# Kernel tuning notes

Measured on AMD Instinct MI355X. Metric: run time of the kernel, lower is better.

## Reference

```python
import jax, jax.numpy as jnp
import numpy as np

EPS = 1e-5

def sage_conv(x, edge_index, w_l, b_l, w_r):
    # PyG SAGEConv with mean aggregation: lin_l(mean of source-neighbor feats per dst) + lin_r(x)
    n = x.shape[0]
    src, dst = edge_index[0], edge_index[1]
    agg = jax.ops.segment_sum(x[src], dst, num_segments=n)  # [N, d]
    deg = jax.ops.segment_sum(jnp.ones((edge_index.shape[1],), x.dtype), dst, num_segments=n)
    agg = agg / jnp.maximum(deg, 1.0)[:, None]
    return agg @ w_l + b_l + x @ w_r

def batchnorm_eval(x, gamma, beta, mean, var):
    return (x - mean) * (gamma * jax.lax.rsqrt(var + EPS)) + beta

def setup_inputs() -> dict:
    key = jax.random.key(0)
    ks = jax.random.split(key, 12)
    N, E, D, H, O = 10000, 160000, 512, 512, 256
    inp = {
        'x': jax.random.normal(ks[0], (N, D), jnp.float32),
        'edge_index': jax.random.randint(ks[1], (2, E), 0, N, jnp.int32),
        'w_l1': jax.random.normal(ks[2], (D, H), jnp.float32) * (1.0 / np.sqrt(D)),
        'b1': jnp.zeros((H,), jnp.float32),
        'w_r1': jax.random.normal(ks[3], (D, H), jnp.float32) * (1.0 / np.sqrt(D)),
        'bn1_gamma': jnp.ones((H,), jnp.float32),
        'bn1_beta': jnp.zeros((H,), jnp.float32),
        'bn1_mean': jax.random.normal(ks[4], (H,), jnp.float32) * 0.1,
        'bn1_var': jax.random.uniform(ks[5], (H,), jnp.float32, 0.5, 1.5),
        'w_l2': jax.random.normal(ks[6], (H, H), jnp.float32) * (1.0 / np.sqrt(H)),
        'b2': jnp.zeros((H,), jnp.float32),
        'w_r2': jax.random.normal(ks[7], (H, H), jnp.float32) * (1.0 / np.sqrt(H)),
        'bn2_gamma': jnp.ones((H,), jnp.float32),
        'bn2_beta': jnp.zeros((H,), jnp.float32),
        'bn2_mean': jax.random.normal(ks[8], (H,), jnp.float32) * 0.1,
        'bn2_var': jax.random.uniform(ks[9], (H,), jnp.float32, 0.5, 1.5),
        'w_l3': jax.random.normal(ks[10], (H, O), jnp.float32) * (1.0 / np.sqrt(H)),
        'b3': jnp.zeros((O,), jnp.float32),
        'w_r3': jax.random.normal(ks[11], (H, O), jnp.float32) * (1.0 / np.sqrt(H)),
    }
    return inp

def reference(x, edge_index, w_l1, b1, w_r1, bn1_gamma, bn1_beta, bn1_mean, bn1_var,
              w_l2, b2, w_r2, bn2_gamma, bn2_beta, bn2_mean, bn2_var,
              w_l3, b3, w_r3):
    # Layer 1: SAGEConv -> BN (eval) -> ReLU (dropout is identity in eval)
    h = sage_conv(x, edge_index, w_l1, b1, w_r1)
    h = jax.nn.relu(batchnorm_eval(h, bn1_gamma, bn1_beta, bn1_mean, bn1_var))
    # Layer 2
    h = sage_conv(h, edge_index, w_l2, b2, w_r2)
    h = jax.nn.relu(batchnorm_eval(h, bn2_gamma, bn2_beta, bn2_mean, bn2_var))
    # Layer 3 (no BN/ReLU)
    return sage_conv(h, edge_index, w_l3, b3, w_r3)
```

## Files before the change

kernel.cpp:

```cpp
#include <hip/hip_runtime.h>

#define NNODE 10000
#define NEDGE 160000

using frag8 = __attribute__((ext_vector_type(8))) short;
using f32x4 = __attribute__((ext_vector_type(4))) float;

__device__ __forceinline__ unsigned short f2bf(float f) {
    union { float f; unsigned u; } v; v.f = f;
    unsigned r = (v.u + 0x7fffu + ((v.u >> 16) & 1u)) >> 16;
    return (unsigned short)r;
}
__device__ __forceinline__ float bf2f(unsigned short s) {
    union { unsigned u; float f; } v; v.u = ((unsigned)s) << 16; return v.f;
}

__global__ __launch_bounds__(1024) void k_scan(const int* __restrict__ deg,
                                               int* __restrict__ rs,
                                               int* __restrict__ cur, int n, int total) {
    const int tid = threadIdx.x;
    const int CH = 10;
    const int base = tid * CH;
    int vals[CH];
    int tsum = 0;
#pragma unroll
    for (int j = 0; j < CH; j++) {
        int v = (base + j < n) ? deg[base + j] : 0;
        vals[j] = v; tsum += v;
    }
    const int lane = tid & 63, wid = tid >> 6;
    int x = tsum;
#pragma unroll
    for (int d = 1; d < 64; d <<= 1) {
        int y = __shfl_up(x, d, 64);
        if (lane >= d) x += y;
    }
    __shared__ int wt[16];
    if (lane == 63) wt[wid] = x;
    __syncthreads();
    if (tid == 0) {
        int c = 0;
#pragma unroll
        for (int k = 0; k < 16; k++) { int t = wt[k]; wt[k] = c; c += t; }
    }
    __syncthreads();
    int run = wt[wid] + x - tsum;
#pragma unroll
    for (int j = 0; j < CH; j++) {
        if (base + j < n) { rs[base + j] = run; cur[base + j] = run; }
        run += vals[j];
    }
    if (tid == 0) rs[n] = total;
}

__global__ void k_fill(const int* __restrict__ src, const int* __restrict__ dst,
                       int E, int* __restrict__ cur, int* __restrict__ csr) {
    int e = blockIdx.x * 256 + threadIdx.x;
    if (e < E) {
        int p = atomicAdd(&cur[dst[e]], 1);
        csr[p] = src[e];
    }
}

__global__ __launch_bounds__(256) void k_prep(
    const float* __restrict__ x, unsigned short* __restrict__ xb,
    const float* __restrict__ wl1, const float* __restrict__ wr1,
    const float* __restrict__ wl2, const float* __restrict__ wr2,
    const float* __restrict__ wl3, const float* __restrict__ wr3,
    unsigned short* __restrict__ bt1, unsigned short* __restrict__ bt2,
    unsigned short* __restrict__ bt3,
    const float* __restrict__ b1, const float* __restrict__ g1, const float* __restrict__ be1,
    const float* __restrict__ m1, const float* __restrict__ v1,
    const float* __restrict__ b2, const float* __restrict__ g2, const float* __restrict__ be2,
    const float* __restrict__ m2, const float* __restrict__ v2,
    const float* __restrict__ b3,
    float* __restrict__ sc1, float* __restrict__ sh1,
    float* __restrict__ sc2, float* __restrict__ sh2,
    float* __restrict__ sc3, float* __restrict__ sh3,
    const int* __restrict__ dstI, int* __restrict__ deg) {
    const int b = blockIdx.x, tid = threadIdx.x;
    if (b < 5000) {
        int i = b * 256 + tid;
        float4 f = ((const float4*)x)[i];
        ushort4 o;
        o.x = f2bf(f.x); o.y = f2bf(f.y); o.z = f2bf(f.z); o.w = f2bf(f.w);
        ((ushort4*)xb)[i] = o;
        return;
    }
    if (b >= 6281) {
        int e = (b - 6281) * 256 + tid;
        if (e < NEDGE) atomicAdd(&deg[dstI[e]], 1);
        return;
    }
    if (b == 6280) {
        for (int t = tid; t < 512; t += 256) {
            float s1 = g1[t] * rsqrtf(v1[t] + 1e-5f);
            sc1[t] = s1; sh1[t] = (b1[t] - m1[t]) * s1 + be1[t];
            float s2 = g2[t] * rsqrtf(v2[t] + 1e-5f);
            sc2[t] = s2; sh2[t] = (b2[t] - m2[t]) * s2 + be2[t];
        }
        if (tid < 256) { sc3[tid] = 1.0f; sh3[tid] = b3[tid]; }
        return;
    }
    __shared__ float t[32][33];
    int tj = b - 5000;
    const float* srcp; unsigned short* dstp; int C, koff, ntilesN;
    if (tj < 1024) {
        int job = tj >> 8; int tile = tj & 255; C = 512; ntilesN = 16;
        srcp = (job == 0) ? wl1 : (job == 1) ? wr1 : (job == 2) ? wl2 : wr2;
        dstp = (job < 2) ? bt1 : bt2; koff = (job & 1) * 512;
        tj = tile;
    } else {
        int jj = tj - 1024; int job = jj >> 7; int tile = jj & 127; C = 256; ntilesN = 8;
        srcp = (job == 0) ? wl3 : wr3; dstp = bt3; koff = job * 512;
        tj = tile;
    }
    int k0 = (tj / ntilesN) * 32, c0 = (tj % ntilesN) * 32;
    int tx = tid & 31, ty = tid >> 5;
#pragma unroll
    for (int q = 0; q < 4; q++)
        t[ty + 8 * q][tx] = srcp[(long)(k0 + ty + 8 * q) * C + c0 + tx];
    __syncthreads();
#pragma unroll
    for (int q = 0; q < 4; q++)
        dstp[(long)(c0 + ty + 8 * q) * 1024 + koff + k0 + tx] = f2bf(t[tx][ty + 8 * q]);
}

__global__ __launch_bounds__(64) void k_agg(const unsigned short* __restrict__ S,
                                            const int* __restrict__ rs, const int* __restrict__ csr,
                                            unsigned short* __restrict__ outb) {
    const int n = blockIdx.x;
    const int c = blockIdx.y * 128 + threadIdx.x * 2;
    const int s = rs[n], e = rs[n + 1];
    float a0 = 0.f, a1 = 0.f;
    int i = s;
    for (; i + 4 <= e; i += 4) {
        int r0 = csr[i], r1 = csr[i + 1], r2 = csr[i + 2], r3 = csr[i + 3];
        unsigned u0 = *(const unsigned*)(S + (long)r0 * 512 + c);
        unsigned u1 = *(const unsigned*)(S + (long)r1 * 512 + c);
        unsigned u2 = *(const unsigned*)(S + (long)r2 * 512 + c);
        unsigned u3 = *(const unsigned*)(S + (long)r3 * 512 + c);
        a0 += bf2f((unsigned short)(u0 & 0xffffu)); a1 += bf2f((unsigned short)(u0 >> 16));
        a0 += bf2f((unsigned short)(u1 & 0xffffu)); a1 += bf2f((unsigned short)(u1 >> 16));
        a0 += bf2f((unsigned short)(u2 & 0xffffu)); a1 += bf2f((unsigned short)(u2 >> 16));
        a0 += bf2f((unsigned short)(u3 & 0xffffu)); a1 += bf2f((unsigned short)(u3 >> 16));
    }
    for (; i < e; i++) {
        unsigned u = *(const unsigned*)(S + (long)csr[i] * 512 + c);
        a0 += bf2f((unsigned short)(u & 0xffffu)); a1 += bf2f((unsigned short)(u >> 16));
    }
    const int cnt = e - s;
    const float inv = 1.f / (float)(cnt > 1 ? cnt : 1);
    unsigned o = (unsigned)f2bf(a0 * inv) | ((unsigned)f2bf(a1 * inv) << 16);
    *(unsigned*)(outb + (long)n * 512 + c) = o;
}

template <int MODE, int NOUT>
__global__ __launch_bounds__(256) void k_gemm(const unsigned short* __restrict__ Agg,
                                              const unsigned short* __restrict__ Self,
                                              const unsigned short* __restrict__ Bt,
                                              const float* __restrict__ sc, const float* __restrict__ sh,
                                              unsigned short* __restrict__ hout, float* __restrict__ fout,
                                              int M) {
    __shared__ __align__(16) short As[2][128 * 64];
    __shared__ __align__(16) short Bs[2][64 * 64];
    const int tid = threadIdx.x;
    const int m0 = blockIdx.x * 128, n0 = blockIdx.y * 64;
    const int w = tid >> 6, lane = tid & 63;
    const int wm = (w >> 1) * 64, wn = (w & 1) * 32;
    const int fr = lane & 15;
    const int fq = lane >> 4;
    const int sw = fr & 7;

    const int srow = w * 8 + (lane >> 3);
    const int scol = (((lane & 7) ^ (lane >> 3)) * 8);
    const int ldsOff = w * 8 * 64;

    f32x4 acc[4][2];
#pragma unroll
    for (int i = 0; i < 4; i++)
#pragma unroll
        for (int j = 0; j < 2; j++)
#pragma unroll
            for (int r = 0; r < 4; r++) acc[i][j][r] = 0.f;

    auto issue = [&](int t, int buf) {
        const short* abase = (const short*)((t < 8) ? Agg : Self);
        const int kk = (t & 7) * 64;
        const int k0 = t * 64;
#pragma unroll
        for (int cch = 0; cch < 4; cch++)
            __builtin_amdgcn_global_load_lds(
                (const __attribute__((address_space(1))) void*)(abase + (long)(m0 + cch * 32 + srow) * 512 + kk + scol),
                (__attribute__((address_space(3))) void*)(&As[buf][ldsOff + cch * 32 * 64]), 16, 0, 0);
#pragma unroll
        for (int cch = 0; cch < 2; cch++)
            __builtin_amdgcn_global_load_lds(
                (const __attribute__((address_space(1))) void*)((const short*)Bt + (long)(n0 + cch * 32 + srow) * 1024 + k0 + scol),
                (__attribute__((address_space(3))) void*)(&Bs[buf][ldsOff + cch * 32 * 64]), 16, 0, 0);
    };

    issue(0, 0);
#pragma unroll
    for (int t = 0; t < 16; t++) {
        const int cur = t & 1;
        __syncthreads();
        if (t < 15) issue(t + 1, cur ^ 1);
#pragma unroll
        for (int ks = 0; ks < 2; ks++) {
            frag8 af[4], bf[2];
#pragma unroll
            for (int i = 0; i < 4; i++)
                af[i] = *(const frag8*)(&As[cur][(wm + i * 16 + fr) * 64 + (((ks * 4 + fq) ^ sw) * 8)]);
#pragma unroll
            for (int j = 0; j < 2; j++)
                bf[j] = *(const frag8*)(&Bs[cur][(wn + j * 16 + fr) * 64 + (((ks * 4 + fq) ^ sw) * 8)]);
#pragma unroll
            for (int i = 0; i < 4; i++)
#pragma unroll
                for (int j = 0; j < 2; j++)
                    acc[i][j] = __builtin_amdgcn_mfma_f32_16x16x32_bf16(af[i], bf[j], acc[i][j], 0, 0, 0);
        }
        __syncthreads();
    }

    float scj[2], shj[2];
#pragma unroll
    for (int j = 0; j < 2; j++) {
        int col = n0 + wn + j * 16 + fr;
        scj[j] = sc[col]; shj[j] = sh[col];
    }
#pragma unroll
    for (int i = 0; i < 4; i++) {
        int rowb = m0 + wm + i * 16 + fq * 4;
#pragma unroll
        for (int j = 0; j < 2; j++) {
            int col = n0 + wn + j * 16 + fr;
#pragma unroll
            for (int r = 0; r < 4; r++) {
                int row = rowb + r;
                if (row < M) {
                    float y = acc[i][j][r] * scj[j] + shj[j];
                    if constexpr (MODE == 0) {
                        y = fmaxf(y, 0.f);
                        hout[(long)row * 512 + col] = f2bf(y);
                    } else {
                        fout[(long)row * NOUT + col] = y;
                    }
                }
            }
        }
    }
}

extern "C" void kernel_launch(void* const* d_in, const int* in_sizes, int n_in,
                              void* d_out, int out_size, void* d_ws, size_t ws_size,
                              hipStream_t stream) {
    const float* x    = (const float*)d_in[0];
    const int*   ei   = (const int*)d_in[1];
    const float* w_l1 = (const float*)d_in[2];
    const float* b1   = (const float*)d_in[3];
    const float* w_r1 = (const float*)d_in[4];
    const float* g1   = (const float*)d_in[5];
    const float* be1  = (const float*)d_in[6];
    const float* m1   = (const float*)d_in[7];
    const float* v1   = (const float*)d_in[8];
    const float* w_l2 = (const float*)d_in[9];
    const float* b2   = (const float*)d_in[10];
    const float* w_r2 = (const float*)d_in[11];
    const float* g2   = (const float*)d_in[12];
    const float* be2  = (const float*)d_in[13];
    const float* m2   = (const float*)d_in[14];
    const float* v2   = (const float*)d_in[15];
    const float* w_l3 = (const float*)d_in[16];
    const float* b3   = (const float*)d_in[17];
    const float* w_r3 = (const float*)d_in[18];
    float* out = (float*)d_out;

    const int N = NNODE, E = NEDGE;
    const int* srcI = ei;
    const int* dstI = ei + E;

    char* w = (char*)d_ws;
    auto alloc = [&](size_t bytes) { void* p = (void*)w; w += (bytes + 255) & ~(size_t)255; return p; };
    int* deg = (int*)alloc((size_t)N * 4);
    int* rs  = (int*)alloc((size_t)(N + 1) * 4);
    int* cur = (int*)alloc((size_t)N * 4);
    int* csr = (int*)alloc((size_t)E * 4);
    unsigned short* xb   = (unsigned short*)alloc((size_t)N * 512 * 2);
    unsigned short* bt1  = (unsigned short*)alloc((size_t)512 * 1024 * 2);
    unsigned short* bt2  = (unsigned short*)alloc((size_t)512 * 1024 * 2);
    unsigned short* bt3  = (unsigned short*)alloc((size_t)256 * 1024 * 2);
    float* sc1 = (float*)alloc(512 * 4); float* sh1 = (float*)alloc(512 * 4);
    float* sc2 = (float*)alloc(512 * 4); float* sh2 = (float*)alloc(512 * 4);
    float* sc3 = (float*)alloc(256 * 4); float* sh3 = (float*)alloc(256 * 4);
    unsigned short* agg_a = (unsigned short*)alloc((size_t)N * 512 * 2);
    unsigned short* h1    = (unsigned short*)alloc((size_t)N * 512 * 2);
    unsigned short* h2    = (unsigned short*)alloc((size_t)N * 512 * 2);
    (void)alloc(256 * 1024);

    hipMemsetAsync(deg, 0, (size_t)N * 4, stream);
    k_prep<<<6906, 256, 0, stream>>>(x, xb, w_l1, w_r1, w_l2, w_r2, w_l3, w_r3,
                                     bt1, bt2, bt3,
                                     b1, g1, be1, m1, v1, b2, g2, be2, m2, v2, b3,
                                     sc1, sh1, sc2, sh2, sc3, sh3, dstI, deg);
    k_scan<<<1, 1024, 0, stream>>>(deg, rs, cur, N, E);
    k_fill<<<(E + 255) / 256, 256, 0, stream>>>(srcI, dstI, E, cur, csr);

    dim3 g12((N + 127) / 128, 8);
    dim3 g3((N + 127) / 128, 4);
    dim3 ga(N, 4);

    k_agg<<<ga, 64, 0, stream>>>(xb, rs, csr, agg_a);
    k_gemm<0, 512><<<g12, 256, 0, stream>>>(agg_a, xb, bt1, sc1, sh1, h1, nullptr, N);
    k_agg<<<ga, 64, 0, stream>>>(h1, rs, csr, agg_a);
    k_gemm<0, 512><<<g12, 256, 0, stream>>>(agg_a, h1, bt2, sc2, sh2, h2, nullptr, N);
    k_agg<<<ga, 64, 0, stream>>>(h2, rs, csr, agg_a);
    k_gemm<1, 256><<<g3, 256, 0, stream>>>(agg_a, h2, bt3, sc3, sh3, nullptr, out, N);
}
```

Before: 272.5 us.

## Fuse all stages into one persistent cooperative kernel with grid syncs

Replaces the memset plus nine separate launches (prep, scan, fill, three aggregations, three GEMMs) with a single persistent cooperative kernel of 512 blocks that loops over work and separates phases with grid-wide barriers. Degree counting moves into its own phase after zeroing, the scan runs on one 256-thread block, and GEMM tiles are remapped in groups of 8 row tiles per column tile for L2 reuse. This removes launch gaps and per-kernel tail effects, but in exchange it limits parallelism to the resident grid and adds grid.sync overhead. The scan is now serialized on a single block while the rest of the grid waits.

After: 964.7 us. 254% more time.

```diff
diff --git a/kernel.cpp b/kernel.cpp
--- a/kernel.cpp
+++ b/kernel.cpp
@@ -1,7 +1,11 @@
 #include <hip/hip_runtime.h>
+#include <hip/hip_cooperative_groups.h>
+namespace cg = cooperative_groups;
 
 #define NNODE 10000
 #define NEDGE 160000
+#define GRID  512
+#define NTHR  256
 
 using frag8 = __attribute__((ext_vector_type(8))) short;
 using f32x4 = __attribute__((ext_vector_type(4))) float;
@@ -15,237 +19,153 @@
     union { unsigned u; float f; } v; v.u = ((unsigned)s) << 16; return v.f;
 }
 
-__global__ __launch_bounds__(1024) void k_scan(const int* __restrict__ deg,
-                                               int* __restrict__ rs,
-                                               int* __restrict__ cur, int n, int total) {
+struct P {
+    const float* x; const int* srcI; const int* dstI;
+    const float *wl1, *wr1, *wl2, *wr2, *wl3, *wr3;
+    const float *b1, *g1, *be1, *m1, *v1;
+    const float *b2, *g2, *be2, *m2, *v2;
+    const float *b3;
+    int *deg, *rs, *cur, *csr;
+    unsigned short *xb, *bt1, *bt2, *bt3, *agg, *h1, *h2;
+    float *sc1, *sh1, *sc2, *sh2, *sc3, *sh3;
+    float* out;
+};
+
+__device__ __forceinline__ void agg_phase(const unsigned short* __restrict__ S,
+                                          const int* __restrict__ rs,
+                                          const int* __restrict__ csr,
+                                          unsigned short* __restrict__ outb) {
+    const int lane = threadIdx.x & 63;
+    const int wv = blockIdx.x * 4 + (threadIdx.x >> 6);
+    for (int job = wv; job < 4 * NNODE; job += GRID * 4) {
+        const int pass = job / NNODE;
+        const int n = job - pass * NNODE;
+        const int c = pass * 128 + lane * 2;
+        const int s = rs[n], e = rs[n + 1];
+        float a0 = 0.f, a1 = 0.f;
+        int i = s;
+        for (; i + 4 <= e; i += 4) {
+            int r0 = csr[i], r1 = csr[i + 1], r2 = csr[i + 2], r3 = csr[i + 3];
+            unsigned u0 = *(const unsigned*)(S + (long)r0 * 512 + c);
+            unsigned u1 = *(const unsigned*)(S + (long)r1 * 512 + c);
+            unsigned u2 = *(const unsigned*)(S + (long)r2 * 512 + c);
+            unsigned u3 = *(const unsigned*)(S + (long)r3 * 512 + c);
+            a0 += bf2f((unsigned short)(u0 & 0xffffu)); a1 += bf2f((unsigned short)(u0 >> 16));
+            a0 += bf2f((unsigned short)(u1 & 0xffffu)); a1 += bf2f((unsigned short)(u1 >> 16));
+            a0 += bf2f((unsigned short)(u2 & 0xffffu)); a1 += bf2f((unsigned short)(u2 >> 16));
+            a0 += bf2f((unsigned short)(u3 & 0xffffu)); a1 += bf2f((unsigned short)(u3 >> 16));
+        }
+        for (; i < e; i++) {
+            unsigned u = *(const unsigned*)(S + (long)csr[i] * 512 + c);
+            a0 += bf2f((unsigned short)(u & 0xffffu)); a1 += bf2f((unsigned short)(u >> 16));
+        }
+        const int cnt = e - s;
+        const float inv = 1.f / (float)(cnt > 1 ? cnt : 1);
+        unsigned o = (unsigned)f2bf(a0 * inv) | ((unsigned)f2bf(a1 * inv) << 16);
+        *(unsigned*)(outb + (long)n * 512 + c) = o;
+    }
+}
+
+__device__ __forceinline__ void gemm_phase(const unsigned short* __restrict__ Agg,
+                                           const unsigned short* __restrict__ Self,
+                                           const unsigned short* __restrict__ Bt,
+                                           const float* __restrict__ sc, const float* __restrict__ sh,
+                                           unsigned short* __restrict__ hout, float* __restrict__ fout,
+                                           int NT, int qsh, int mode,
+                                           short* __restrict__ AsB, short* __restrict__ BsB) {
     const int tid = threadIdx.x;
-    const int CH = 10;
-    const int base = tid * CH;
-    int vals[CH];
-    int tsum = 0;
-#pragma unroll
-    for (int j = 0; j < CH; j++) {
-        int v = (base + j < n) ? deg[base + j] : 0;
-        vals[j] = v; tsum += v;
-    }
-    const int lane = tid & 63, wid = tid >> 6;
-    int x = tsum;
-#pragma unroll
-    for (int d = 1; d < 64; d <<= 1) {
-        int y = __shfl_up(x, d, 64);
-        if (lane >= d) x += y;
-    }
-    __shared__ int wt[16];
-    if (lane == 63) wt[wid] = x;
-    __syncthreads();
-    if (tid == 0) {
-        int c = 0;
-#pragma unroll
-        for (int k = 0; k < 16; k++) { int t = wt[k]; wt[k] = c; c += t; }
-    }
-    __syncthreads();
-    int run = wt[wid] + x - tsum;
-#pragma unroll
-    for (int j = 0; j < CH; j++) {
-        if (base + j < n) { rs[base + j] = run; cur[base + j] = run; }
-        run += vals[j];
-    }
-    if (tid == 0) rs[n] = total;
-}
-
-__global__ void k_fill(const int* __restrict__ src, const int* __restrict__ dst,
-                       int E, int* __restrict__ cur, int* __restrict__ csr) {
-    int e = blockIdx.x * 256 + threadIdx.x;
-    if (e < E) {
-        int p = atomicAdd(&cur[dst[e]], 1);
-        csr[p] = src[e];
-    }
-}
-
-__global__ __launch_bounds__(256) void k_prep(
-    const float* __restrict__ x, unsigned short* __restrict__ xb,
-    const float* __restrict__ wl1, const float* __restrict__ wr1,
-    const float* __restrict__ wl2, const float* __restrict__ wr2,
-    const float* __restrict__ wl3, const float* __restrict__ wr3,
-    unsigned short* __restrict__ bt1, unsigned short* __restrict__ bt2,
-    unsigned short* __restrict__ bt3,
-    const float* __restrict__ b1, const float* __restrict__ g1, const float* __restrict__ be1,
-    const float* __restrict__ m1, const float* __restrict__ v1,
-    const float* __restrict__ b2, const float* __restrict__ g2, const float* __restrict__ be2,
-    const float* __restrict__ m2, const float* __restrict__ v2,
-    const float* __restrict__ b3,
-    float* __restrict__ sc1, float* __restrict__ sh1,
-    float* __restrict__ sc2, float* __restrict__ sh2,
-    float* __restrict__ sc3, float* __restrict__ sh3,
-    const int* __restrict__ dstI, int* __restrict__ deg) {
-    const int b = blockIdx.x, tid = threadIdx.x;
-    if (b < 5000) {
-        int i = b * 256 + tid;
-        float4 f = ((const float4*)x)[i];
-        ushort4 o;
-        o.x = f2bf(f.x); o.y = f2bf(f.y); o.z = f2bf(f.z); o.w = f2bf(f.w);
-        ((ushort4*)xb)[i] = o;
-        return;
-    }
-    if (b >= 6281) {
-        int e = (b - 6281) * 256 + tid;
-        if (e < NEDGE) atomicAdd(&deg[dstI[e]], 1);
-        return;
-    }
-    if (b == 6280) {
-        for (int t = tid; t < 512; t += 256) {
-            float s1 = g1[t] * rsqrtf(v1[t] + 1e-5f);
-            sc1[t] = s1; sh1[t] = (b1[t] - m1[t]) * s1 + be1[t];
-            float s2 = g2[t] * rsqrtf(v2[t] + 1e-5f);
-            sc2[t] = s2; sh2[t] = (b2[t] - m2[t]) * s2 + be2[t];
-        }
-        if (tid < 256) { sc3[tid] = 1.0f; sh3[tid] = b3[tid]; }
-        return;
-    }
-    __shared__ float t[32][33];
-    int tj = b - 5000;
-    const float* srcp; unsigned short* dstp; int C, koff, ntilesN;
-    if (tj < 1024) {
-        int job = tj >> 8; int tile = tj & 255; C = 512; ntilesN = 16;
-        srcp = (job == 0) ? wl1 : (job == 1) ? wr1 : (job == 2) ? wl2 : wr2;
-        dstp = (job < 2) ? bt1 : bt2; koff = (job & 1) * 512;
-        tj = tile;
-    } else {
-        int jj = tj - 1024; int job = jj >> 7; int tile = jj & 127; C = 256; ntilesN = 8;
-        srcp = (job == 0) ? wl3 : wr3; dstp = bt3; koff = job * 512;
-        tj = tile;
-    }
-    int k0 = (tj / ntilesN) * 32, c0 = (tj % ntilesN) * 32;
-    int tx = tid & 31, ty = tid >> 5;
-#pragma unroll
-    for (int q = 0; q < 4; q++)
-        t[ty + 8 * q][tx] = srcp[(long)(k0 + ty + 8 * q) * C + c0 + tx];
-    __syncthreads();
-#pragma unroll
-    for (int q = 0; q < 4; q++)
-        dstp[(long)(c0 + ty + 8 * q) * 1024 + koff + k0 + tx] = f2bf(t[tx][ty + 8 * q]);
-}
-
-__global__ __launch_bounds__(64) void k_agg(const unsigned short* __restrict__ S,
-                                            const int* __restrict__ rs, const int* __restrict__ csr,
-                                            unsigned short* __restrict__ outb) {
-    const int n = blockIdx.x;
-    const int c = blockIdx.y * 128 + threadIdx.x * 2;
-    const int s = rs[n], e = rs[n + 1];
-    float a0 = 0.f, a1 = 0.f;
-    int i = s;
-    for (; i + 4 <= e; i += 4) {
-        int r0 = csr[i], r1 = csr[i + 1], r2 = csr[i + 2], r3 = csr[i + 3];
-        unsigned u0 = *(const unsigned*)(S + (long)r0 * 512 + c);
-        unsigned u1 = *(const unsigned*)(S + (long)r1 * 512 + c);
-        unsigned u2 = *(const unsigned*)(S + (long)r2 * 512 + c);
-        unsigned u3 = *(const unsigned*)(S + (long)r3 * 512 + c);
-        a0 += bf2f((unsigned short)(u0 & 0xffffu)); a1 += bf2f((unsigned short)(u0 >> 16));
-        a0 += bf2f((unsigned short)(u1 & 0xffffu)); a1 += bf2f((unsigned short)(u1 >> 16));
-        a0 += bf2f((unsigned short)(u2 & 0xffffu)); a1 += bf2f((unsigned short)(u2 >> 16));
-        a0 += bf2f((unsigned short)(u3 & 0xffffu)); a1 += bf2f((unsigned short)(u3 >> 16));
-    }
-    for (; i < e; i++) {
-        unsigned u = *(const unsigned*)(S + (long)csr[i] * 512 + c);
-        a0 += bf2f((unsigned short)(u & 0xffffu)); a1 += bf2f((unsigned short)(u >> 16));
-    }
-    const int cnt = e - s;
-    const float inv = 1.f / (float)(cnt > 1 ? cnt : 1);
-    unsigned o = (unsigned)f2bf(a0 * inv) | ((unsigned)f2bf(a1 * inv) << 16);
-    *(unsigned*)(outb + (long)n * 512 + c) = o;
-}
-
-template <int MODE, int NOUT>
-__global__ __launch_bounds__(256) void k_gemm(const unsigned short* __restrict__ Agg,
-                                              const unsigned short* __restrict__ Self,
-                                              const unsigned short* __restrict__ Bt,
-                                              const float* __restrict__ sc, const float* __restrict__ sh,
-                                              unsigned short* __restrict__ hout, float* __restrict__ fout,
-                                              int M) {
-    __shared__ __align__(16) short As[2][128 * 64];
-    __shared__ __align__(16) short Bs[2][64 * 64];
-    const int tid = threadIdx.x;
-    const int m0 = blockIdx.x * 128, n0 = blockIdx.y * 64;
     const int w = tid >> 6, lane = tid & 63;
     const int wm = (w >> 1) * 64, wn = (w & 1) * 32;
-    const int fr = lane & 15;
-    const int fq = lane >> 4;
-    const int sw = fr & 7;
-
+    const int fr = lane & 15, fq = lane >> 4, sw = fr & 7;
     const int srow = w * 8 + (lane >> 3);
     const int scol = (((lane & 7) ^ (lane >> 3)) * 8);
     const int ldsOff = w * 8 * 64;
-
-    f32x4 acc[4][2];
-#pragma unroll
-    for (int i = 0; i < 4; i++)
-#pragma unroll
-        for (int j = 0; j < 2; j++)
-#pragma unroll
-            for (int r = 0; r < 4; r++) acc[i][j][r] = 0.f;
-
-    auto issue = [&](int t, int buf) {
-        const short* abase = (const short*)((t < 8) ? Agg : Self);
-        const int kk = (t & 7) * 64;
-        const int k0 = t * 64;
-#pragma unroll
-        for (int cch = 0; cch < 4; cch++)
-            __builtin_amdgcn_global_load_lds(
-                (const __attribute__((address_space(1))) void*)(abase + (long)(m0 + cch * 32 + srow) * 512 + kk + scol),
-                (__attribute__((address_space(3))) void*)(&As[buf][ldsOff + cch * 32 * 64]), 16, 0, 0);
-#pragma unroll
-        for (int cch = 0; cch < 2; cch++)
-            __builtin_amdgcn_global_load_lds(
-                (const __attribute__((address_space(1))) void*)((const short*)Bt + (long)(n0 + cch * 32 + srow) * 1024 + k0 + scol),
-                (__attribute__((address_space(3))) void*)(&Bs[buf][ldsOff + cch * 32 * 64]), 16, 0, 0);
-    };
-
-    issue(0, 0);
-#pragma unroll
-    for (int t = 0; t < 16; t++) {
-        const int cur = t & 1;
-        __syncthreads();
-        if (t < 15) issue(t + 1, cur ^ 1);
-#pragma unroll
-        for (int ks = 0; ks < 2; ks++) {
-            frag8 af[4], bf[2];
-#pragma unroll
-            for (int i = 0; i < 4; i++)
-                af[i] = *(const frag8*)(&As[cur][(wm + i * 16 + fr) * 64 + (((ks * 4 + fq) ^ sw) * 8)]);
+    const int vtiles = 80 * NT;
+
+    for (int vb = blockIdx.x; vb < vtiles; vb += GRID) {
+        const int X = vb & 7;
+        const int q = (vb >> 3) & (NT - 1);
+        const int g = vb >> qsh;
+        const int m0 = (g * 8 + X) * 128;
+        if (m0 >= NNODE) continue;
+        const int n0 = q * 64;
+
+        f32x4 acc[4][2];
+#pragma unroll
+        for (int i = 0; i < 4; i++)
 #pragma unroll
             for (int j = 0; j < 2; j++)
-                bf[j] = *(const frag8*)(&Bs[cur][(wn + j * 16 + fr) * 64 + (((ks * 4 + fq) ^ sw) * 8)]);
-#pragma unroll
-            for (int i = 0; i < 4; i++)
+#pragma unroll
+                for (int r = 0; r < 4; r++) acc[i][j][r] = 0.f;
+
+        auto issue = [&](int t, int buf) {
+            const short* abase = (const short*)((t < 8) ? Agg : Self);
+            const int kk = (t & 7) * 64;
+            const int k0 = t * 64;
+            short* asD = AsB + buf * 128 * 64 + ldsOff;
+            short* bsD = BsB + buf * 64 * 64 + ldsOff;
+#pragma unroll
+            for (int cch = 0; cch < 4; cch++)
+                __builtin_amdgcn_global_load_lds(
+                    (const __attribute__((address_space(1))) void*)(abase + (long)(m0 + cch * 32 + srow) * 512 + kk + scol),
+                    (__attribute__((address_space(3))) void*)(asD + cch * 32 * 64), 16, 0, 0);
+#pragma unroll
+            for (int cch = 0; cch < 2; cch++)
+                __builtin_amdgcn_global_load_lds(
+                    (const __attribute__((address_space(1))) void*)((const short*)Bt + (long)(n0 + cch * 32 + srow) * 1024 + k0 + scol),
+                    (__attribute__((address_space(3))) void*)(bsD + cch * 32 * 64), 16, 0, 0);
+        };
+
+        issue(0, 0);
+#pragma unroll
+        for (int t = 0; t < 16; t++) {
+            const int cur = t & 1;
+            __syncthreads();
+            if (t < 15) issue(t + 1, cur ^ 1);
+            const short* AsC = AsB + cur * 128 * 64;
+            const short* BsC = BsB + cur * 64 * 64;
+#pragma unroll
+            for (int ks = 0; ks < 2; ks++) {
+                frag8 af[4], bf[2];
+#pragma unroll
+                for (int i = 0; i < 4; i++)
+                    af[i] = *(const frag8*)(AsC + (wm + i * 16 + fr) * 64 + (((ks * 4 + fq) ^ sw) * 8));
 #pragma unroll
                 for (int j = 0; j < 2; j++)
-                    acc[i][j] = __builtin_amdgcn_mfma_f32_16x16x32_bf16(af[i], bf[j], acc[i][j], 0, 0, 0);
-        }
-        __syncthreads();
-    }
-
-    float scj[2], shj[2];
-#pragma unroll
-    for (int j = 0; j < 2; j++) {
-        int col = n0 + wn + j * 16 + fr;
-        scj[j] = sc[col]; shj[j] = sh[col];
-    }
-#pragma unroll
-    for (int i = 0; i < 4; i++) {
-        int rowb = m0 + wm + i * 16 + fq * 4;
+                    bf[j] = *(const frag8*)(BsC + (wn + j * 16 + fr) * 64 + (((ks * 4 + fq) ^ sw) * 8));
+#pragma unroll
+                for (int i = 0; i < 4; i++)
+#pragma unroll
+                    for (int j = 0; j < 2; j++)
+                        acc[i][j] = __builtin_amdgcn_mfma_f32_16x16x32_bf16(af[i], bf[j], acc[i][j], 0, 0, 0);
+            }
+            __syncthreads();
+        }
+
+        float scj[2], shj[2];
 #pragma unroll
         for (int j = 0; j < 2; j++) {
             int col = n0 + wn + j * 16 + fr;
-#pragma unroll
-            for (int r = 0; r < 4; r++) {
-                int row = rowb + r;
-                if (row < M) {
-                    float y = acc[i][j][r] * scj[j] + shj[j];
-                    if constexpr (MODE == 0) {
-                        y = fmaxf(y, 0.f);
-                        hout[(long)row * 512 + col] = f2bf(y);
-                    } else {
-                        fout[(long)row * NOUT + col] = y;
+            scj[j] = sc[col]; shj[j] = sh[col];
+        }
+        const int NOUT = NT * 64;
+#pragma unroll
+        for (int i = 0; i < 4; i++) {
+            int rowb = m0 + wm + i * 16 + fq * 4;
+#pragma unroll
+            for (int j = 0; j < 2; j++) {
+                int col = n0 + wn + j * 16 + fr;
+#pragma unroll
+                for (int r = 0; r < 4; r++) {
+                    int row = rowb + r;
+                    if (row < NNODE) {
+                        float y = acc[i][j][r] * scj[j] + shj[j];
+                        if (mode == 0) {
+                            y = fmaxf(y, 0.f);
+                            hout[(long)row * 512 + col] = f2bf(y);
+                        } else {
+                            fout[(long)row * NOUT + col] = y;
+                        }
                     }
                 }
             }
@@ -253,68 +173,148 @@
     }
 }
 
+__global__ __launch_bounds__(NTHR, 2) void mega(P p) {
+    __shared__ __align__(16) short As[2 * 128 * 64];
+    __shared__ __align__(16) short Bs[2 * 64 * 64];
+    __shared__ float tt[32][33];
+    __shared__ int wt[4];
+    cg::grid_group grid = cg::this_grid();
+    const int b = blockIdx.x, tid = threadIdx.x;
+    const int gt = b * NTHR + tid;
+
+    if (gt < NNODE) p.deg[gt] = 0;
+    for (int j = b; j < 5000; j += GRID) {
+        int i = j * 256 + tid;
+        float4 f = ((const float4*)p.x)[i];
+        ushort4 o;
+        o.x = f2bf(f.x); o.y = f2bf(f.y); o.z = f2bf(f.z); o.w = f2bf(f.w);
+        ((ushort4*)p.xb)[i] = o;
+    }
+    if (b == GRID - 1) {
+        for (int t = tid; t < 512; t += NTHR) {
+            float s1 = p.g1[t] * rsqrtf(p.v1[t] + 1e-5f);
+            p.sc1[t] = s1; p.sh1[t] = (p.b1[t] - p.m1[t]) * s1 + p.be1[t];
+            float s2 = p.g2[t] * rsqrtf(p.v2[t] + 1e-5f);
+            p.sc2[t] = s2; p.sh2[t] = (p.b2[t] - p.m2[t]) * s2 + p.be2[t];
+        }
+        if (tid < 256) { p.sc3[tid] = 1.0f; p.sh3[tid] = p.b3[tid]; }
+    }
+    for (int tj = b; tj < 1280; tj += GRID) {
+        const float* srcp; unsigned short* dstp; int C, koff, ntilesN, tl;
+        if (tj < 1024) {
+            int job = tj >> 8; tl = tj & 255; C = 512; ntilesN = 16;
+            srcp = (job == 0) ? p.wl1 : (job == 1) ? p.wr1 : (job == 2) ? p.wl2 : p.wr2;
+            dstp = (job < 2) ? p.bt1 : p.bt2; koff = (job & 1) * 512;
+        } else {
+            int jj = tj - 1024; int job = jj >> 7; tl = jj & 127; C = 256; ntilesN = 8;
+            srcp = (job == 0) ? p.wl3 : p.wr3; dstp = p.bt3; koff = job * 512;
+        }
+        int k0 = (tl / ntilesN) * 32, c0 = (tl % ntilesN) * 32;
+        int tx = tid & 31, ty = tid >> 5;
+        __syncthreads();
+#pragma unroll
+        for (int q = 0; q < 4; q++)
+            tt[ty + 8 * q][tx] = srcp[(long)(k0 + ty + 8 * q) * C + c0 + tx];
+        __syncthreads();
+#pragma unroll
+        for (int q = 0; q < 4; q++)
+            dstp[(long)(c0 + ty + 8 * q) * 1024 + koff + k0 + tx] = f2bf(tt[tx][ty + 8 * q]);
+    }
+    grid.sync();
+
+    for (int e = gt; e < NEDGE; e += GRID * NTHR)
+        atomicAdd(&p.deg[p.dstI[e]], 1);
+    grid.sync();
+
+    if (b == 0) {
+        const int CH = 40;
+        const int base = tid * CH;
+        int tsum = 0;
+        for (int j = 0; j < CH; j++) {
+            int idx = base + j;
+            tsum += (idx < NNODE) ? p.deg[idx] : 0;
+        }
+        const int lane = tid & 63, wid = tid >> 6;
+        int xx = tsum;
+#pragma unroll
+        for (int d = 1; d < 64; d <<= 1) {
+            int y = __shfl_up(xx, d, 64);
+            if (lane >= d) xx += y;
+        }
+        if (lane == 63) wt[wid] = xx;
+        __syncthreads();
+        if (tid == 0) {
+            int c = 0;
+#pragma unroll
+            for (int k = 0; k < 4; k++) { int t2 = wt[k]; wt[k] = c; c += t2; }
+        }
+        __syncthreads();
+        int run = wt[wid] + xx - tsum;
+        for (int j = 0; j < CH; j++) {
+            int idx = base + j;
+            if (idx < NNODE) {
+                p.rs[idx] = run; p.cur[idx] = run;
+                run += p.deg[idx];
+            }
+        }
+        if (tid == 0) p.rs[NNODE] = NEDGE;
+    }
+    grid.sync();
+
+    for (int e = gt; e < NEDGE; e += GRID * NTHR) {
+        int pos = atomicAdd(&p.cur[p.dstI[e]], 1);
+        p.csr[pos] = p.srcI[e];
+    }
+    grid.sync();
+
+    agg_phase(p.xb, p.rs, p.csr, p.agg);
+    grid.sync();
+    gemm_phase(p.agg, p.xb, p.bt1, p.sc1, p.sh1, p.h1, nullptr, 8, 6, 0, As, Bs);
+    grid.sync();
+    agg_phase(p.h1, p.rs, p.csr, p.agg);
+    grid.sync();
+    gemm_phase(p.agg, p.h1, p.bt2, p.sc2, p.sh2, p.h2, nullptr, 8, 6, 0, As, Bs);
+    grid.sync();
+    agg_phase(p.h2, p.rs, p.csr, p.agg);
+    grid.sync();
+    gemm_phase(p.agg, p.h2, p.bt3, p.sc3, p.sh3, nullptr, p.out, 4, 5, 1, As, Bs);
+}
+
 extern "C" void kernel_launch(void* const* d_in, const int* in_sizes, int n_in,
                               void* d_out, int out_size, void* d_ws, size_t ws_size,
                               hipStream_t stream) {
-    const float* x    = (const float*)d_in[0];
-    const int*   ei   = (const int*)d_in[1];
-    const float* w_l1 = (const float*)d_in[2];
-    const float* b1   = (const float*)d_in[3];
-    const float* w_r1 = (const float*)d_in[4];
-    const float* g1   = (const float*)d_in[5];
-    const float* be1  = (const float*)d_in[6];
-    const float* m1   = (const float*)d_in[7];
-    const float* v1   = (const float*)d_in[8];
-    const float* w_l2 = (const float*)d_in[9];
-    const float* b2   = (const float*)d_in[10];
-    const float* w_r2 = (const float*)d_in[11];
-    const float* g2   = (const float*)d_in[12];
-    const float* be2  = (const float*)d_in[13];
-    const float* m2   = (const float*)d_in[14];
-    const float* v2   = (const float*)d_in[15];
-    const float* w_l3 = (const float*)d_in[16];
-    const float* b3   = (const float*)d_in[17];
-    const float* w_r3 = (const float*)d_in[18];
-    float* out = (float*)d_out;
-
-    const int N = NNODE, E = NEDGE;
-    const int* srcI = ei;
-    const int* dstI = ei + E;
+    P p;
+    p.x    = (const float*)d_in[0];
+    const int* ei = (const int*)d_in[1];
+    p.srcI = ei; p.dstI = ei + NEDGE;
+    p.wl1 = (const float*)d_in[2];  p.b1 = (const float*)d_in[3];  p.wr1 = (const float*)d_in[4];
+    p.g1 = (const float*)d_in[5];   p.be1 = (const float*)d_in[6];
+    p.m1 = (const float*)d_in[7];   p.v1 = (const float*)d_in[8];
+    p.wl2 = (const float*)d_in[9];  p.b2 = (const float*)d_in[10]; p.wr2 = (const float*)d_in[11];
+    p.g2 = (const float*)d_in[12];  p.be2 = (const float*)d_in[13];
+    p.m2 = (const float*)d_in[14];  p.v2 = (const float*)d_in[15];
+    p.wl3 = (const float*)d_in[16]; p.b3 = (const float*)d_in[17]; p.wr3 = (const float*)d_in[18];
+    p.out = (float*)d_out;
 
     char* w = (char*)d_ws;
-    auto alloc = [&](size_t bytes) { void* p = (void*)w; w += (bytes + 255) & ~(size_t)255; return p; };
-    int* deg = (int*)alloc((size_t)N * 4);
-    int* rs  = (int*)alloc((size_t)(N + 1) * 4);
-    int* cur = (int*)alloc((size_t)N * 4);
-    int* csr = (int*)alloc((size_t)E * 4);
-    unsigned short* xb   = (unsigned short*)alloc((size_t)N * 512 * 2);
-    unsigned short* bt1  = (unsigned short*)alloc((size_t)512 * 1024 * 2);
-    unsigned short* bt2  = (unsigned short*)alloc((size_t)512 * 1024 * 2);
-    unsigned short* bt3  = (unsigned short*)alloc((size_t)256 * 1024 * 2);
-    float* sc1 = (float*)alloc(512 * 4); float* sh1 = (float*)alloc(512 * 4);
-    float* sc2 = (float*)alloc(512 * 4); float* sh2 = (float*)alloc(512 * 4);
-    float* sc3 = (float*)alloc(256 * 4); float* sh3 = (float*)alloc(256 * 4);
-    unsigned short* agg_a = (unsigned short*)alloc((size_t)N * 512 * 2);
-    unsigned short* h1    = (unsigned short*)alloc((size_t)N * 512 * 2);
-    unsigned short* h2    = (unsigned short*)alloc((size_t)N * 512 * 2);
+    auto alloc = [&](size_t bytes) { void* q = (void*)w; w += (bytes + 255) & ~(size_t)255; return q; };
+    p.deg = (int*)alloc((size_t)NNODE * 4);
+    p.rs  = (int*)alloc((size_t)(NNODE + 1) * 4);
+    p.cur = (int*)alloc((size_t)NNODE * 4);
+    p.csr = (int*)alloc((size_t)NEDGE * 4);
+    p.xb  = (unsigned short*)alloc((size_t)NNODE * 512 * 2);
+    p.bt1 = (unsigned short*)alloc((size_t)512 * 1024 * 2);
+    p.bt2 = (unsigned short*)alloc((size_t)512 * 1024 * 2);
+    p.bt3 = (unsigned short*)alloc((size_t)256 * 1024 * 2);
+    p.sc1 = (float*)alloc(512 * 4); p.sh1 = (float*)alloc(512 * 4);
+    p.sc2 = (float*)alloc(512 * 4); p.sh2 = (float*)alloc(512 * 4);
+    p.sc3 = (float*)alloc(256 * 4); p.sh3 = (float*)alloc(256 * 4);
+    p.agg = (unsigned short*)alloc((size_t)NNODE * 512 * 2);
+    p.h1  = (unsigned short*)alloc((size_t)NNODE * 512 * 2);
+    p.h2  = (unsigned short*)alloc((size_t)NNODE * 512 * 2);
     (void)alloc(256 * 1024);
 
-    hipMemsetAsync(deg, 0, (size_t)N * 4, stream);
-    k_prep<<<6906, 256, 0, stream>>>(x, xb, w_l1, w_r1, w_l2, w_r2, w_l3, w_r3,
-                                     bt1, bt2, bt3,
-                                     b1, g1, be1, m1, v1, b2, g2, be2, m2, v2, b3,
-                                     sc1, sh1, sc2, sh2, sc3, sh3, dstI, deg);
-    k_scan<<<1, 1024, 0, stream>>>(deg, rs, cur, N, E);
-    k_fill<<<(E + 255) / 256, 256, 0, stream>>>(srcI, dstI, E, cur, csr);
-
-    dim3 g12((N + 127) / 128, 8);
-    dim3 g3((N + 127) / 128, 4);
-    dim3 ga(N, 4);
-
-    k_agg<<<ga, 64, 0, stream>>>(xb, rs, csr, agg_a);
-    k_gemm<0, 512><<<g12, 256, 0, stream>>>(agg_a, xb, bt1, sc1, sh1, h1, nullptr, N);
-    k_agg<<<ga, 64, 0, stream>>>(h1, rs, csr, agg_a);
-    k_gemm<0, 512><<<g12, 256, 0, stream>>>(agg_a, h1, bt2, sc2, sh2, h2, nullptr, N);
-    k_agg<<<ga, 64, 0, stream>>>(h2, rs, csr, agg_a);
-    k_gemm<1, 256><<<g3, 256, 0, stream>>>(agg_a, h2, bt3, sc3, sh3, nullptr, out, N);
-}
+    void* args[] = { &p };
+    hipLaunchCooperativeKernel(reinterpret_cast<void*>(mega), dim3(GRID), dim3(NTHR),
+                               args, 0, stream);
+}
```
